# Kernel optimization log

Measured on AMD Instinct MI355X. Metric: run time of the kernel, lower is better.

The kernel has to match this reference:

```python
import jax, jax.numpy as jnp
import numpy as np

N, E, B = 30000, 240000, 64
F, H, T = 64, 4, 3
BOT = 256


def _gat_layer(x, e_src, e_dst, lin_w, att_src, att_dst, bias):
    # x: [N, in]; lin_w: [in, H*F]; att_*: [H, F]; bias: [H*F]
    xs = (x @ lin_w).reshape(N, H, F)                     # [N,H,F]
    a_src = jnp.einsum('nhf,hf->nh', xs, att_src)         # [N,H]
    a_dst = jnp.einsum('nhf,hf->nh', xs, att_dst)
    logits = jax.nn.leaky_relu(a_src[e_src] + a_dst[e_dst], negative_slope=0.2)  # [E2,H]
    m = jax.ops.segment_max(logits, e_dst, num_segments=N)        # softmax over in-edges per dst
    ex = jnp.exp(logits - m[e_dst])
    denom = jax.ops.segment_sum(ex, e_dst, num_segments=N)
    alpha = ex / (denom[e_dst] + 1e-16)                   # [E2,H]
    msg = alpha[:, :, None] * xs[e_src]                   # [E2,H,F]
    out = jax.ops.segment_sum(msg, e_dst, num_segments=N).reshape(N, H * F)
    return out + bias


def setup_inputs() -> dict:
    key = jax.random.key(0)
    ks = jax.random.split(key, 20)
    s = 0.1
    inp = {
        'street_feature': jax.random.normal(ks[0], (N, 5), jnp.float32),
        'edge_index': jax.random.randint(ks[1], (2, E), 0, N, dtype=jnp.int64),
        'batch': jnp.sort(jax.random.randint(ks[2], (N,), 0, B, dtype=jnp.int64)),
        'bbox_w': jax.random.normal(ks[3], (5, F), jnp.float32) * s,
        'bbox_b': jnp.zeros((F,), jnp.float32),
        'lin_w0': jax.random.normal(ks[4], (F, H * F), jnp.float32) * s,
        'att_src0': jax.random.normal(ks[5], (H, F), jnp.float32) * s,
        'att_dst0': jax.random.normal(ks[6], (H, F), jnp.float32) * s,
        'bias0': jnp.zeros((H * F,), jnp.float32),
        'lin_w1': jax.random.normal(ks[7], (H * F, H * F), jnp.float32) * s,
        'att_src1': jax.random.normal(ks[8], (H, F), jnp.float32) * s,
        'att_dst1': jax.random.normal(ks[9], (H, F), jnp.float32) * s,
        'bias1': jnp.zeros((H * F,), jnp.float32),
        'lin_w2': jax.random.normal(ks[10], (H * F, H * F), jnp.float32) * s,
        'att_src2': jax.random.normal(ks[11], (H, F), jnp.float32) * s,
        'att_dst2': jax.random.normal(ks[12], (H, F), jnp.float32) * s,
        'bias2': jnp.zeros((H * F,), jnp.float32),
        'agg_w': jax.random.normal(ks[13], (F * (1 + H * T), BOT), jnp.float32) * s,
        'agg_b': jnp.zeros((BOT,), jnp.float32),
    }
    return inp


def reference(street_feature, edge_index, batch,
              bbox_w, bbox_b,
              lin_w0, att_src0, att_dst0, bias0,
              lin_w1, att_src1, att_dst1, bias1,
              lin_w2, att_src2, att_dst2, bias2,
              agg_w, agg_b):
    # add self-loops (PyG GATConv default add_self_loops=True)
    loop = jnp.arange(N, dtype=edge_index.dtype)
    e_src = jnp.concatenate([edge_index[0], loop])
    e_dst = jnp.concatenate([edge_index[1], loop])

    x = jax.nn.relu(street_feature @ bbox_w + bbox_b)            # [N,F]
    g = [jax.ops.segment_max(x, batch, num_segments=B)]          # global max pool

    layers = [(lin_w0, att_src0, att_dst0, bias0),
              (lin_w1, att_src1, att_dst1, bias1),
              (lin_w2, att_src2, att_dst2, bias2)]
    for lw, asrc, adst, b in layers:
        x = jax.nn.relu(_gat_layer(x, e_src, e_dst, lw, asrc, adst, b))  # [N,H*F]
        g.append(jax.ops.segment_max(x, batch, num_segments=B))

    g_embed = jnp.concatenate(g, axis=1)                          # [B, F*(1+H*T)]
    return g_embed @ agg_w + agg_b                                # [B, BOT]
```

## Files before the change

kernel.cpp:

```cpp
#include <hip/hip_runtime.h>
#include <hip/hip_bf16.h>

#define N_NODES 30000
#define N_EDGES 240000
#define NB      64
#define FDIM    64
#define NH      4
#define HF      256
#define E2      (N_EDGES + N_NODES)
#define GCOLS   832
#define BOTD    256
#define DEGCAP  64
#define PSPLIT  16
#define FSPLIT  8

typedef __hip_bfloat16 bf16;
typedef __attribute__((ext_vector_type(8))) short short8;
typedef __attribute__((ext_vector_type(4))) float f32x4;
typedef __attribute__((ext_vector_type(4))) unsigned short u16x4;

#define LDA 40

__device__ __forceinline__ float b2f(bf16 v) { return __bfloat162float(v); }
__device__ __forceinline__ float bits2f(unsigned short u) {
    return __uint_as_float(((unsigned int)u) << 16);
}

#define ENC_B   7500
#define ADJ_B   1055
#define BOFF_B  118
#define WT0 (HF * FDIM)
#define WT1 (WT0 + HF * HF)
#define WT2 (WT1 + HF * HF)
#define WCONV_B 576
#define GZ_B    208
#define OZ_B    64
#define PRO_B   (ENC_B + ADJ_B + BOFF_B + WCONV_B + GZ_B + OZ_B)

__global__ __launch_bounds__(256) void prologue_kernel(
        const float* __restrict__ sf, const float* __restrict__ bw,
        const float* __restrict__ bb, bf16* __restrict__ xenc,
        const int* __restrict__ esrc, const int* __restrict__ edst,
        int* __restrict__ deg, unsigned short* __restrict__ adj,
        const int* __restrict__ batch, int* __restrict__ boff,
        const float* __restrict__ w0, const float* __restrict__ w1,
        const float* __restrict__ w2, bf16* __restrict__ wT,
        float* __restrict__ g, float* __restrict__ dout) {
    int b = blockIdx.x, t = threadIdx.x;
    if (b < ENC_B) {
        int i = b * 256 + t;
        int n = i >> 6, f = i & 63;
        float acc = bb[f];
#pragma unroll
        for (int k = 0; k < 5; ++k)
            acc += sf[n * 5 + k] * bw[k * FDIM + f];
        xenc[i] = __float2bfloat16(fmaxf(acc, 0.f));
    } else if (b < ENC_B + ADJ_B) {
        int e = (b - ENC_B) * 256 + t;
        if (e >= E2) return;
        int s, d;
        if (e < N_EDGES) { s = esrc[e]; d = edst[e]; }
        else             { s = d = e - N_EDGES; }
        int pos = atomicAdd(&deg[d], 1);
        if (pos < DEGCAP) adj[d * DEGCAP + pos] = (unsigned short)s;
    } else if (b < ENC_B + ADJ_B + BOFF_B) {
        int n = (b - ENC_B - ADJ_B) * 256 + t;
        if (n >= N_NODES) return;
        int b1 = batch[n];
        int b0 = (n == 0) ? -1 : batch[n - 1];
        for (int x = b0 + 1; x <= b1; ++x) boff[x] = n;
        if (n == N_NODES - 1)
            for (int x = b1 + 1; x <= NB; ++x) boff[x] = N_NODES;
    } else if (b < ENC_B + ADJ_B + BOFF_B + WCONV_B) {
        int i = (b - ENC_B - ADJ_B - BOFF_B) * 256 + t;
        if (i < WT0) {
            int n = i / FDIM, k = i - n * FDIM;
            wT[i] = __float2bfloat16(w0[k * HF + n]);
        } else if (i < WT1) {
            int j = i - WT0, n = j >> 8, k = j & 255;
            wT[i] = __float2bfloat16(w1[k * HF + n]);
        } else if (i < WT2) {
            int j = i - WT1, n = j >> 8, k = j & 255;
            wT[i] = __float2bfloat16(w2[k * HF + n]);
        }
    } else if (b < ENC_B + ADJ_B + BOFF_B + WCONV_B + GZ_B) {
        g[(b - ENC_B - ADJ_B - BOFF_B - WCONV_B) * 256 + t] = 0.f;
    } else {
        dout[(b - ENC_B - ADJ_B - BOFF_B - WCONV_B - GZ_B) * 256 + t] = 0.f;
    }
}

template <int K>
__global__ __launch_bounds__(256) void gemm_mfma_kernel(
        const bf16* __restrict__ xb, const bf16* __restrict__ wT,
        bf16* __restrict__ y, const float* __restrict__ asrc,
        const float* __restrict__ adst, float* __restrict__ a_s,
        float* __restrict__ a_d) {
    __shared__ short sA[64 * LDA];
    __shared__ short sB[256 * LDA];
    int t = threadIdx.x, w = t >> 6, l = t & 63;
    int q = l >> 4, m = l & 15;
    int n0 = blockIdx.x * 64;
    const short* xg = (const short*)xb;
    const short* wg = (const short*)wT;
    int ar = t >> 2, ac = t & 3;
    f32x4 acc[4][4];
#pragma unroll
    for (int rt = 0; rt < 4; ++rt)
#pragma unroll
        for (int ct = 0; ct < 4; ++ct)
            acc[rt][ct] = (f32x4){0.f, 0.f, 0.f, 0.f};

    short8 pa = {0, 0, 0, 0, 0, 0, 0, 0};
    short8 pb[4];
    if (n0 + ar < N_NODES) pa = *(const short8*)&xg[(long)(n0 + ar) * K + ac * 8];
#pragma unroll
    for (int u = 0; u < 4; ++u)
        pb[u] = *(const short8*)&wg[(long)t * K + u * 8];

#pragma unroll
    for (int k0 = 0; k0 < K; k0 += 32) {
        *(short8*)&sA[ar * LDA + ac * 8] = pa;
        {
            short* dst = &sB[t * LDA];
#pragma unroll
            for (int u = 0; u < 4; ++u) *(short8*)&dst[u * 8] = pb[u];
        }
        __syncthreads();
        if (k0 + 32 < K) {
            pa = (short8){0, 0, 0, 0, 0, 0, 0, 0};
            if (n0 + ar < N_NODES)
                pa = *(const short8*)&xg[(long)(n0 + ar) * K + k0 + 32 + ac * 8];
#pragma unroll
            for (int u = 0; u < 4; ++u)
                pb[u] = *(const short8*)&wg[(long)t * K + k0 + 32 + u * 8];
        }
        short8 af[4], bfr[4];
#pragma unroll
        for (int rt = 0; rt < 4; ++rt)
            af[rt] = *(const short8*)&sA[(16 * rt + m) * LDA + q * 8];
#pragma unroll
        for (int ct = 0; ct < 4; ++ct)
            bfr[ct] = *(const short8*)&sB[(64 * w + 16 * ct + m) * LDA + q * 8];
#pragma unroll
        for (int rt = 0; rt < 4; ++rt)
#pragma unroll
            for (int ct = 0; ct < 4; ++ct)
                acc[rt][ct] = __builtin_amdgcn_mfma_f32_16x16x32_bf16(
                    af[rt], bfr[ct], acc[rt][ct], 0, 0, 0);
        __syncthreads();
    }

#pragma unroll
    for (int rt = 0; rt < 4; ++rt)
#pragma unroll
        for (int reg = 0; reg < 4; ++reg) {
            int row = n0 + 16 * rt + 4 * q + reg;
            if (row < N_NODES) {
#pragma unroll
                for (int ct = 0; ct < 4; ++ct)
                    y[(long)row * HF + 64 * w + 16 * ct + m] =
                        __float2bfloat16(acc[rt][ct][reg]);
            }
        }
    float vs[4], vd[4];
#pragma unroll
    for (int ct = 0; ct < 4; ++ct) {
        vs[ct] = asrc[64 * w + 16 * ct + m];
        vd[ct] = adst[64 * w + 16 * ct + m];
    }
#pragma unroll
    for (int rt = 0; rt < 4; ++rt)
#pragma unroll
        for (int reg = 0; reg < 4; ++reg) {
            float ps = 0.f, pd = 0.f;
#pragma unroll
            for (int ct = 0; ct < 4; ++ct) {
                ps += acc[rt][ct][reg] * vs[ct];
                pd += acc[rt][ct][reg] * vd[ct];
            }
#pragma unroll
            for (int mask = 1; mask <= 8; mask <<= 1) {
                ps += __shfl_xor(ps, mask, 64);
                pd += __shfl_xor(pd, mask, 64);
            }
            if (m == 0) {
                int row = n0 + 16 * rt + 4 * q + reg;
                if (row < N_NODES) {
                    a_s[row * NH + w] = ps;
                    a_d[row * NH + w] = pd;
                }
            }
        }
}

#define EXP_S (DEGCAP + 4)
__global__ __launch_bounds__(256) void agg_kernel(
        const unsigned short* __restrict__ adj, const int* __restrict__ deg,
        const bf16* __restrict__ xs, const float* __restrict__ a_s,
        const float* __restrict__ a_d, const float* __restrict__ bias,
        bf16* __restrict__ xout) {
    int w = threadIdx.x >> 6, l = threadIdx.x & 63;
    int n = blockIdx.x * 4 + w;
    __shared__ unsigned short s_src_all[4][DEGCAP];
    __shared__ float s_ex_all[4][NH][EXP_S];
    unsigned short* s_src = s_src_all[w];
    float (*s_ex)[EXP_S] = s_ex_all[w];
    int dn = min(deg[n], DEGCAP);
    int src_l = 0;
    if (l < dn) {
        src_l = adj[n * DEGCAP + l];
        s_src[l] = (unsigned short)src_l;
    }
    f32x4 ad4 = *(const f32x4*)&a_d[n * NH];
    float ex[NH];
    if (l < dn) {
        f32x4 as4 = *(const f32x4*)&a_s[src_l * NH];
#pragma unroll
        for (int h = 0; h < NH; ++h) {
            float a = as4[h] + ad4[h];
            a = (a > 0.f) ? a : 0.2f * a;
            ex[h] = __expf(a);
        }
    } else {
#pragma unroll
        for (int h = 0; h < NH; ++h) ex[h] = 0.f;
    }
#pragma unroll
    for (int h = 0; h < NH; ++h) {
        float s = ex[h];
#pragma unroll
        for (int off = 32; off > 0; off >>= 1) s += __shfl_xor(s, off, 64);
        s_ex[h][l] = ex[h] * (1.f / (s + 1e-16f));
    }
    __builtin_amdgcn_wave_barrier();
    int hh = l >> 4;
    const unsigned short* xg = (const unsigned short*)xs;
    f32x4 acc = {0.f, 0.f, 0.f, 0.f};
    int k = 0;
    for (; k + 1 < dn; k += 2) {
        int s0 = s_src[k], s1 = s_src[k + 1];
        float a0 = s_ex[hh][k], a1 = s_ex[hh][k + 1];
        u16x4 v0 = *(const u16x4*)&xg[(long)s0 * HF + 4 * l];
        u16x4 v1 = *(const u16x4*)&xg[(long)s1 * HF + 4 * l];
#pragma unroll
        for (int j = 0; j < 4; ++j) {
            acc[j] += a0 * bits2f(v0[j]);
            acc[j] += a1 * bits2f(v1[j]);
        }
    }
    if (k < dn) {
        int s0 = s_src[k];
        float a0 = s_ex[hh][k];
        u16x4 v0 = *(const u16x4*)&xg[(long)s0 * HF + 4 * l];
#pragma unroll
        for (int j = 0; j < 4; ++j) acc[j] += a0 * bits2f(v0[j]);
    }
    f32x4 b4 = *(const f32x4*)&bias[4 * l];
    u16x4 o;
#pragma unroll
    for (int j = 0; j < 4; ++j) {
        bf16 ob = __float2bfloat16(fmaxf(acc[j] + b4[j], 0.f));
        o[j] = *reinterpret_cast<unsigned short*>(&ob);
    }
    *(u16x4*)((unsigned short*)xout + (long)n * HF + 4 * l) = o;
}

__global__ __launch_bounds__(256) void pool256_kernel(const bf16* __restrict__ x,
                                                      const int* __restrict__ boff,
                                                      unsigned int* __restrict__ g, int goff) {
    int b = blockIdx.x / PSPLIT, part = blockIdx.x % PSPLIT;
    int t = threadIdx.x, w = t >> 6, l = t & 63;
    int s = boff[b], e = boff[b + 1];
    int chunk = (e - s + PSPLIT - 1) / PSPLIT;
    int cs = s + part * chunk, ce = min(cs + chunk, e);
    if (cs >= ce) return;
    __shared__ f32x4 sm[256];
    const unsigned short* xg = (const unsigned short*)x;
    f32x4 v = {0.f, 0.f, 0.f, 0.f};
    for (int n = cs + w; n < ce; n += 4) {
        u16x4 u = *(const u16x4*)&xg[(long)n * HF + 4 * l];
#pragma unroll
        for (int j = 0; j < 4; ++j) v[j] = fmaxf(v[j], bits2f(u[j]));
    }
    sm[t] = v;
    __syncthreads();
    const float* smf = (const float*)sm;
    float m = fmaxf(fmaxf(smf[t], smf[256 + t]), fmaxf(smf[512 + t], smf[768 + t]));
    atomicMax(&g[b * GCOLS + goff + t], __float_as_uint(m));
}

__global__ __launch_bounds__(256) void pool64_kernel(const bf16* __restrict__ x,
                                                     const int* __restrict__ boff,
                                                     unsigned int* __restrict__ g) {
    int b = blockIdx.x / PSPLIT, part = blockIdx.x % PSPLIT;
    int t = threadIdx.x, c = t & 63, r = t >> 6;
    int s = boff[b], e = boff[b + 1];
    int chunk = (e - s + PSPLIT - 1) / PSPLIT;
    int cs = s + part * chunk, ce = min(cs + chunk, e);
    __shared__ float sm[256];
    float v = 0.f;
    for (int n = cs + r; n < ce; n += 4)
        v = fmaxf(v, b2f(x[(long)n * FDIM + c]));
    sm[t] = v;
    __syncthreads();
    if (t < 64 && cs < ce) {
        float m = fmaxf(fmaxf(sm[t], sm[t + 64]), fmaxf(sm[t + 128], sm[t + 192]));
        atomicMax(&g[b * GCOLS + t], __float_as_uint(m));
    }
}

__global__ __launch_bounds__(256) void final_kernel(
        const float* __restrict__ g, const float* __restrict__ w,
        const float* __restrict__ b, float* __restrict__ outp) {
    int bb = blockIdx.x & (NB - 1);
    int slice = blockIdx.x >> 6;
    int j = threadIdx.x;
    const int KS = GCOLS / FSPLIT;
    float acc = (slice == 0) ? b[j] : 0.f;
    int k0 = slice * KS;
    for (int k = k0; k < k0 + KS; ++k)
        acc += g[bb * GCOLS + k] * w[k * BOTD + j];
    atomicAdd(&outp[bb * BOTD + j], acc);
}

extern "C" void kernel_launch(void* const* d_in, const int* in_sizes, int n_in,
                              void* d_out, int out_size, void* d_ws, size_t ws_size,
                              hipStream_t stream) {
    const float* sf     = (const float*)d_in[0];
    const int*   eidx   = (const int*)d_in[1];
    const int*   batch  = (const int*)d_in[2];
    const float* bbox_w = (const float*)d_in[3];
    const float* bbox_b = (const float*)d_in[4];
    const float* lin_w[3] = {(const float*)d_in[5],  (const float*)d_in[9],  (const float*)d_in[13]};
    const float* att_s[3] = {(const float*)d_in[6],  (const float*)d_in[10], (const float*)d_in[14]};
    const float* att_d[3] = {(const float*)d_in[7],  (const float*)d_in[11], (const float*)d_in[15]};
    const float* bias[3]  = {(const float*)d_in[8],  (const float*)d_in[12], (const float*)d_in[16]};
    const float* agg_w  = (const float*)d_in[17];
    const float* agg_b  = (const float*)d_in[18];

    const int* esrc = eidx;
    const int* edst = eidx + N_EDGES;

    char* ws = (char*)d_ws;
    bf16* xsb  = (bf16*)ws;  ws += (size_t)N_NODES * HF * 2;
    bf16* xb0  = (bf16*)ws;  ws += (size_t)N_NODES * HF * 2;
    bf16* xb1  = (bf16*)ws;  ws += (size_t)N_NODES * HF * 2;
    bf16* xenc = (bf16*)ws;  ws += (size_t)N_NODES * FDIM * 2;
    float* a_s = (float*)ws; ws += (size_t)N_NODES * NH * 4;
    float* a_d = (float*)ws; ws += (size_t)N_NODES * NH * 4;
    float* g   = (float*)ws; ws += (size_t)NB * GCOLS * 4;
    int*   deg = (int*)ws;   ws += (size_t)N_NODES * 4;
    int*   boff= (int*)ws;   ws += (size_t)(NB + 1) * 4;
    unsigned short* adj = (unsigned short*)ws; ws += (size_t)N_NODES * DEGCAP * 2;
    bf16* wT   = (bf16*)ws;  ws += (size_t)WT2 * 2;

    hipMemsetAsync(deg, 0, (size_t)N_NODES * 4, stream);
    prologue_kernel<<<PRO_B, 256, 0, stream>>>(
        sf, bbox_w, bbox_b, xenc, esrc, edst, deg, adj, batch, boff,
        lin_w[0], lin_w[1], lin_w[2], wT, g, (float*)d_out);
    pool64_kernel<<<NB * PSPLIT, 256, 0, stream>>>(xenc, boff, (unsigned int*)g);

    const bf16* wTl[3] = {wT, wT + WT0, wT + WT1};
    const bf16* xin = xenc;
    bf16* xout = xb0;
    for (int l = 0; l < 3; ++l) {
        if (l == 0)
            gemm_mfma_kernel<FDIM><<<(N_NODES + 63) / 64, 256, 0, stream>>>(
                xin, wTl[l], xsb, att_s[l], att_d[l], a_s, a_d);
        else
            gemm_mfma_kernel<HF><<<(N_NODES + 63) / 64, 256, 0, stream>>>(
                xin, wTl[l], xsb, att_s[l], att_d[l], a_s, a_d);
        agg_kernel<<<N_NODES / 4, 256, 0, stream>>>(adj, deg, xsb, a_s, a_d, bias[l], xout);
        pool256_kernel<<<NB * PSPLIT, 256, 0, stream>>>(xout, boff, (unsigned int*)g, FDIM + l * HF);
        xin = xout;
        xout = (xout == xb0) ? xb1 : xb0;
    }
    final_kernel<<<NB * FSPLIT, 256, 0, stream>>>(g, agg_w, agg_b, (float*)d_out);
}
```

Measured before the change: 283.2 us.

## Use direct global-to-LDS loads with triple-buffered pipeline and XOR swizzle in GEMM

Rewrites the MFMA GEMM main loop to load A and B tiles with global_load_lds straight into a triple-buffered LDS ring, prefetching two stages ahead, using manual vmcnt waits and a single barrier per step. The padded LDS layout is replaced by an XOR-swizzled 32-wide layout to avoid bank conflicts. The goal is to cut register staging, the second barrier and load latency. The out-of-bounds row guard for the last node block is removed, so it may read past the input rows, and it relies on exact vmcnt accounting.

```diff
diff --git a/kernel.cpp b/kernel.cpp
--- a/kernel.cpp
+++ b/kernel.cpp
@@ -18,8 +18,6 @@
 typedef __attribute__((ext_vector_type(8))) short short8;
 typedef __attribute__((ext_vector_type(4))) float f32x4;
 typedef __attribute__((ext_vector_type(4))) unsigned short u16x4;
-
-#define LDA 40
 
 __device__ __forceinline__ float b2f(bf16 v) { return __bfloat162float(v); }
 __device__ __forceinline__ float bits2f(unsigned short u) {
@@ -96,14 +94,35 @@
         bf16* __restrict__ y, const float* __restrict__ asrc,
         const float* __restrict__ adst, float* __restrict__ a_s,
         float* __restrict__ a_d) {
-    __shared__ short sA[64 * LDA];
-    __shared__ short sB[256 * LDA];
+    constexpr int T = K / 32;
+    __shared__ __align__(16) short lds[3 * 10240];
     int t = threadIdx.x, w = t >> 6, l = t & 63;
     int q = l >> 4, m = l & 15;
     int n0 = blockIdx.x * 64;
     const short* xg = (const short*)xb;
     const short* wg = (const short*)wT;
-    int ar = t >> 2, ac = t & 3;
+    int sub = l >> 2;
+    int k2g = (l & 3) ^ ((l >> 3) & 3);
+    int xq  = q ^ ((m >> 1) & 3);
+    long rowA = n0 + 16 * w + sub;
+
+    auto stage = [&](int s) {
+        int bb = s % 3;
+        int k0 = s * 32;
+        __builtin_amdgcn_global_load_lds(
+            (const __attribute__((address_space(1))) void*)&xg[rowA * K + k0 + k2g * 8],
+            (__attribute__((address_space(3))) void*)&lds[bb * 10240 + w * 512],
+            16, 0, 0);
+#pragma unroll
+        for (int u = 0; u < 4; ++u) {
+            int rowB = 64 * w + 16 * u + sub;
+            __builtin_amdgcn_global_load_lds(
+                (const __attribute__((address_space(1))) void*)&wg[(long)rowB * K + k0 + k2g * 8],
+                (__attribute__((address_space(3))) void*)&lds[bb * 10240 + 2048 + (w * 4 + u) * 512],
+                16, 0, 0);
+        }
+    };
+
     f32x4 acc[4][4];
 #pragma unroll
     for (int rt = 0; rt < 4; ++rt)
@@ -111,44 +130,31 @@
         for (int ct = 0; ct < 4; ++ct)
             acc[rt][ct] = (f32x4){0.f, 0.f, 0.f, 0.f};
 
-    short8 pa = {0, 0, 0, 0, 0, 0, 0, 0};
-    short8 pb[4];
-    if (n0 + ar < N_NODES) pa = *(const short8*)&xg[(long)(n0 + ar) * K + ac * 8];
-#pragma unroll
-    for (int u = 0; u < 4; ++u)
-        pb[u] = *(const short8*)&wg[(long)t * K + u * 8];
-
-#pragma unroll
-    for (int k0 = 0; k0 < K; k0 += 32) {
-        *(short8*)&sA[ar * LDA + ac * 8] = pa;
-        {
-            short* dst = &sB[t * LDA];
-#pragma unroll
-            for (int u = 0; u < 4; ++u) *(short8*)&dst[u * 8] = pb[u];
-        }
-        __syncthreads();
-        if (k0 + 32 < K) {
-            pa = (short8){0, 0, 0, 0, 0, 0, 0, 0};
-            if (n0 + ar < N_NODES)
-                pa = *(const short8*)&xg[(long)(n0 + ar) * K + k0 + 32 + ac * 8];
-#pragma unroll
-            for (int u = 0; u < 4; ++u)
-                pb[u] = *(const short8*)&wg[(long)t * K + k0 + 32 + u * 8];
-        }
+    stage(0);
+    if (T > 1) stage(1);
+
+#pragma unroll
+    for (int s = 0; s < T; ++s) {
+        if (s < T - 1) asm volatile("s_waitcnt vmcnt(5)" ::: "memory");
+        else           asm volatile("s_waitcnt vmcnt(0)" ::: "memory");
+        __builtin_amdgcn_s_barrier();
+        __builtin_amdgcn_sched_barrier(0);
+        if (s + 2 < T) stage(s + 2);
+        const short* Ab = &lds[(s % 3) * 10240];
+        const short* Bb = Ab + 2048;
         short8 af[4], bfr[4];
 #pragma unroll
         for (int rt = 0; rt < 4; ++rt)
-            af[rt] = *(const short8*)&sA[(16 * rt + m) * LDA + q * 8];
+            af[rt] = *(const short8*)&Ab[(16 * rt + m) * 32 + xq * 8];
 #pragma unroll
         for (int ct = 0; ct < 4; ++ct)
-            bfr[ct] = *(const short8*)&sB[(64 * w + 16 * ct + m) * LDA + q * 8];
+            bfr[ct] = *(const short8*)&Bb[(64 * w + 16 * ct + m) * 32 + xq * 8];
 #pragma unroll
         for (int rt = 0; rt < 4; ++rt)
 #pragma unroll
             for (int ct = 0; ct < 4; ++ct)
                 acc[rt][ct] = __builtin_amdgcn_mfma_f32_16x16x32_bf16(
                     af[rt], bfr[ct], acc[rt][ct], 0, 0, 0);
-        __syncthreads();
     }
 
 #pragma unroll
```

Measured after the change: 276.4 us. 1.02x faster.
